# Performance work log

Hardware: AMD Instinct MI355X
Metric: run time of the kernel (lower is better)

Reference implementation:

```python
import jax, jax.numpy as jnp
import numpy as np

TRUNC = (24, 24, 24)
OUT = (32, 32, 32)


def setup_inputs() -> dict:
    key = jax.random.key(0)
    x = jax.random.normal(key, (8, 32, 48, 48, 48), dtype=jnp.float32)
    return {"x": x}


def reference(x):
    # "DCT" as implemented in the source: real part of an ortho-normalized 3D FFT
    x_dct = jnp.real(jnp.fft.fftn(x, axes=(2, 3, 4), norm='ortho'))
    # crop to low-frequency corner, zero-pad up to output_size
    x_crop = x_dct[:, :, :TRUNC[0], :TRUNC[1], :TRUNC[2]]
    pad = ((0, 0), (0, 0),
           (0, OUT[0] - TRUNC[0]),
           (0, OUT[1] - TRUNC[1]),
           (0, OUT[2] - TRUNC[2]))
    x_pad = jnp.pad(x_crop, pad)
    # inverse transform on the output_size grid, keep real part
    x_idct = jnp.real(jnp.fft.ifftn(x_pad, axes=(2, 3, 4), norm='ortho'))
    return x_idct
```

## Files before the change

kernel.cpp:

```cpp
#include <hip/hip_runtime.h>
#include <math.h>


#define TWO_PI_48 0.13089969389957470f
#define TWO_PI_32 0.19634954084936207f
#define NORM_F    1.6611664e-05f

typedef _Float16 half8  __attribute__((ext_vector_type(8)));
typedef _Float16 half4v __attribute__((ext_vector_type(4)));
typedef float    f32x4  __attribute__((ext_vector_type(4)));

__device__ _Float16 T1frag[2][3][2][64][8];
__device__ _Float16 T2frag[2][3][2][64][8];
__device__ __align__(16) _Float16 TK2frag[2][4][3][64][8];
__device__ __align__(16) _Float16 MB2frag[2][4][2][64][8];
__device__ __align__(16) _Float16 TB3frag[2][2][2][64][8];

__device__ int g_twdone = 0;

__global__ void k_init_tw() {
  if (g_twdone) return;
  const int idx = blockIdx.x * 256 + threadIdx.x;
  if (idx < 3072) {
    const int j  = idx & 7;
    const int l  = (idx >> 3) & 63;
    const int ks = (idx >> 9) & 1;
    const int t  = idx >> 10;
    const int k  = ks * 32 + (l >> 4) * 8 + j;
    {
      const int m = t * 16 + (l & 15);
      float v = 0.f;
      if (k < 48) {
        const float a = (float)(((m % 24) * k) % 48) * TWO_PI_48;
        v = (m < 24) ? cosf(a) : -sinf(a);
      }
      const _Float16 h = (_Float16)v;
      T1frag[0][t][ks][l][j] = h;
      T1frag[1][t][ks][l][j] = (_Float16)(v - (float)h);
    }
    {
      const int c = t * 16 + (l & 15);
      float v = 0.f;
      if (k < 48) {
        const float a = (float)(((c % 24) * k) % 48) * TWO_PI_48;
        v = (c < 24) ? cosf(a) : sinf(a);
      }
      const _Float16 h = (_Float16)v;
      T2frag[0][t][ks][l][j] = h;
      T2frag[1][t][ks][l][j] = (_Float16)(v - (float)h);
    }
  } else if (idx < 3072 + 6144) {
    const int local = idx - 3072;
    const int j = local & 7, l = (local >> 3) & 63;
    const int rest = local >> 9;
    const int ks = rest % 3, mt = rest / 3;
    const int m   = mt * 16 + (l & 15);
    const int kap = ks * 32 + (l >> 4) * 8 + j;
    const int n1  = kap % 48;
    const bool isVi = kap >= 48;
    const int m1  = m & 31;
    const bool isWi = m >= 32;
    float acc = 0.f;
    for (int k1 = 0; k1 < 24; ++k1) {
      float s32v, c32v, s48v, c48v;
      sincosf((float)((k1 * m1) % 32) * TWO_PI_32, &s32v, &c32v);
      sincosf((float)((k1 * n1) % 48) * TWO_PI_48, &s48v, &c48v);
      acc = fmaf(isWi ? s32v : c32v, isVi ? s48v : c48v, acc);
    }
    const _Float16 h = (_Float16)acc;
    TK2frag[0][mt][ks][l][j] = h;
    TK2frag[1][mt][ks][l][j] = (_Float16)(acc - (float)h);
  } else if (idx < 3072 + 6144 + 4096) {
    const int local = idx - (3072 + 6144);
    const int j = local & 7, l = (local >> 3) & 63;
    const int rest = local >> 9;
    const int ks = rest & 1, mt = rest >> 1;
    const int m   = mt * 16 + (l & 15);
    const int kap = ks * 32 + (l >> 4) * 8 + j;
    float v = 0.f;
    if (kap < 48) {
      const int k2 = kap % 24;
      const int m2 = m & 31;
      float s, c;
      sincosf((float)((k2 * m2) % 32) * TWO_PI_32, &s, &c);
      if (m < 32) v = (kap < 24) ? c : -s;
      else        v = (kap < 24) ? s :  c;
    }
    const _Float16 h = (_Float16)v;
    MB2frag[0][mt][ks][l][j] = h;
    MB2frag[1][mt][ks][l][j] = (_Float16)(v - (float)h);
  } else if (idx < 15360) {
    const int local = idx - (3072 + 6144 + 4096);
    const int j = local & 7, l = (local >> 3) & 63;
    const int rest = local >> 9;
    const int ks = rest & 1, nt = rest >> 1;
    const int m3  = nt * 16 + (l & 15);
    const int kap = ks * 32 + (l >> 4) * 8 + j;
    float v = 0.f;
    if (kap < 48) {
      const int k3 = kap % 24;
      float s, c;
      sincosf((float)((k3 * m3) % 32) * TWO_PI_32, &s, &c);
      v = (kap < 24) ? c : -s;
    }
    const _Float16 h = (_Float16)v;
    TB3frag[0][nt][ks][l][j] = h;
    TB3frag[1][nt][ks][l][j] = (_Float16)(v - (float)h);
  }
}

__device__ inline void split8(const float* qf, half8& h, half8& lo) {
#pragma unroll
  for (int j = 0; j < 8; ++j) {
    const _Float16 hh = (_Float16)qf[j];
    h[j]  = hh;
    lo[j] = (_Float16)(qf[j] - (float)hh);
  }
}

__global__ __launch_bounds__(192) void k_a12_mfma(const float* __restrict__ x,
                                                  float2* __restrict__ V) {
  const int bx   = blockIdx.x;
  const int bc   = blockIdx.y;
  const int tid  = threadIdx.x;
  const int lane = tid & 63;
  const int w    = tid >> 6;

  __shared__ __align__(16) unsigned char arenaX[13824];
  __shared__ __align__(16) unsigned char arenaU[13824];
  _Float16* Xh = (_Float16*)arenaX;
  _Float16* Xl = (_Float16*)(arenaX + 6912);
  float*    D2 = (float*)arenaX;
  _Float16* Uh = (_Float16*)arenaU;
  _Float16* Ul = (_Float16*)(arenaU + 6912);

  half8 t1h[3][2], t1l[3][2];
#pragma unroll
  for (int mt = 0; mt < 3; ++mt)
#pragma unroll
    for (int ks = 0; ks < 2; ++ks) {
      t1h[mt][ks] = *(const half8*)&T1frag[0][mt][ks][lane][0];
      t1l[mt][ks] = *(const half8*)&T1frag[1][mt][ks][lane][0];
    }
  half8 t2h[2], t2l[2];
#pragma unroll
  for (int ks = 0; ks < 2; ++ks) {
    t2h[ks] = *(const half8*)&T2frag[0][w][ks][lane][0];
    t2l[ks] = *(const half8*)&T2frag[1][w][ks][lane][0];
  }

  if (tid < 96) {
    _Float16* p = (tid < 48 ? Uh : Ul) + (tid % 48) * 72 + 48;
    *(half8*)&p[0] = (half8){};
    *(half8*)&p[8] = (half8){};
  }

  const int kb   = (lane >> 4) * 8;
  const int c16  = lane & 15;
  const int k2e  = tid % 24;
  const int k30e = (tid / 24) * 3;

  float4 xr0, xr1, xr2;
  {
    const float4* g4 = (const float4*)(x + ((size_t)(bc * 48 + bx * 2)) * 2304);
    xr0 = g4[tid]; xr1 = g4[tid + 192]; xr2 = g4[tid + 384];
  }

  for (int g = 0; g < 2; ++g) {
    const int n1 = bx * 2 + g;

    {
      const float4 fr[3] = {xr0, xr1, xr2};
#pragma unroll
      for (int jj = 0; jj < 3; ++jj) {
        const int i4 = tid + 192 * jj;
        const int r = i4 / 12, c4 = i4 % 12;
        const float4 f = fr[jj];
        const _Float16 h0 = (_Float16)f.x, h1 = (_Float16)f.y,
                       h2 = (_Float16)f.z, h3 = (_Float16)f.w;
        const half4v hv = {h0, h1, h2, h3};
        const half4v lv = {(_Float16)(f.x - (float)h0), (_Float16)(f.y - (float)h1),
                           (_Float16)(f.z - (float)h2), (_Float16)(f.w - (float)h3)};
        *(half4v*)&Xh[r * 72 + c4 * 4] = hv;
        *(half4v*)&Xl[r * 72 + c4 * 4] = lv;
      }
    }
    if (tid < 96) {
      _Float16* p = (tid < 48 ? Xh : Xl) + (tid % 48) * 72 + 48;
      *(half8*)&p[0] = (half8){};
      *(half8*)&p[8] = (half8){};
    }
    if (g < 1) {
      const float4* g4 = (const float4*)(x + ((size_t)(bc * 48 + n1 + 1)) * 2304);
      xr0 = g4[tid]; xr1 = g4[tid + 192]; xr2 = g4[tid + 384];
    }
    __syncthreads();

    f32x4 acc0 = {}, acc1 = {}, acc2 = {};
#pragma unroll
    for (int ks = 0; ks < 2; ++ks) {
      const half8 bh = *(const half8*)&Xh[(w * 16 + c16) * 72 + ks * 32 + kb];
      const half8 bl = *(const half8*)&Xl[(w * 16 + c16) * 72 + ks * 32 + kb];
#pragma unroll
      for (int mt = 0; mt < 3; ++mt) {
        f32x4& acc = (mt == 0) ? acc0 : (mt == 1) ? acc1 : acc2;
        acc = __builtin_amdgcn_mfma_f32_16x16x32_f16(t1h[mt][ks], bh, acc, 0, 0, 0);
        acc = __builtin_amdgcn_mfma_f32_16x16x32_f16(t1h[mt][ks], bl, acc, 0, 0, 0);
        acc = __builtin_amdgcn_mfma_f32_16x16x32_f16(t1l[mt][ks], bh, acc, 0, 0, 0);
      }
    }

#pragma unroll
    for (int mt = 0; mt < 3; ++mt) {
      const int r0 = mt * 16 + (lane >> 4) * 4;
      const int cc = w * 16 + c16;
      const f32x4 acc = (mt == 0) ? acc0 : (mt == 1) ? acc1 : acc2;
#pragma unroll
      for (int r = 0; r < 4; ++r) {
        const float v = acc[r];
        const _Float16 h = (_Float16)v;
        Uh[(r0 + r) * 72 + cc] = h;
        Ul[(r0 + r) * 72 + cc] = (_Float16)(v - (float)h);
      }
    }
    __syncthreads();

    f32x4 d20 = {}, d21 = {}, d22 = {};
#pragma unroll
    for (int ks = 0; ks < 2; ++ks) {
#pragma unroll
      for (int mt = 0; mt < 3; ++mt) {
        const half8 ah = *(const half8*)&Uh[(mt * 16 + c16) * 72 + ks * 32 + kb];
        const half8 al = *(const half8*)&Ul[(mt * 16 + c16) * 72 + ks * 32 + kb];
        f32x4& acc = (mt == 0) ? d20 : (mt == 1) ? d21 : d22;
        acc = __builtin_amdgcn_mfma_f32_16x16x32_f16(ah, t2h[ks], acc, 0, 0, 0);
        acc = __builtin_amdgcn_mfma_f32_16x16x32_f16(ah, t2l[ks], acc, 0, 0, 0);
        acc = __builtin_amdgcn_mfma_f32_16x16x32_f16(al, t2h[ks], acc, 0, 0, 0);
      }
    }

#pragma unroll
    for (int mt = 0; mt < 3; ++mt) {
      const int r0 = mt * 16 + (lane >> 4) * 4;
      const int cc = w * 16 + c16;
      const f32x4 acc = (mt == 0) ? d20 : (mt == 1) ? d21 : d22;
#pragma unroll
      for (int r = 0; r < 4; ++r) D2[(r0 + r) * 68 + cc] = acc[r];
    }
    __syncthreads();

    float2* Vp = V + (size_t)(bc * 24) * 1152 + (size_t)n1 * 24 + k2e;
#pragma unroll
    for (int q = 0; q < 3; ++q) {
      const int k3 = k30e + q;
      const float grr = D2[k3 * 68 + k2e];
      const float gis = D2[(k3 + 24) * 68 + k2e + 24];
      const float gir = D2[(k3 + 24) * 68 + k2e];
      const float grs = D2[k3 * 68 + k2e + 24];
      Vp[(size_t)k3 * 1152] = make_float2(grr + gis, gir - grs);
    }
    __syncthreads();
  }
}

__global__ __launch_bounds__(192) void k2_mfma(float2* __restrict__ V) {
  const int k3   = blockIdx.x;
  const int byy  = blockIdx.y;
  const int tid  = threadIdx.x;
  const int lane = tid & 63;
  const int w    = tid >> 6;

  __shared__ __align__(16) float Bb[48 * 100];

  half8 kth[4][3], ktl[4][3];
#pragma unroll
  for (int mt = 0; mt < 4; ++mt)
#pragma unroll
    for (int ks = 0; ks < 3; ++ks) {
      kth[mt][ks] = *(const half8*)&TK2frag[0][mt][ks][lane][0];
      ktl[mt][ks] = *(const half8*)&TK2frag[1][mt][ks][lane][0];
    }

  const int kbase = (lane >> 4) * 8;
  const int c16   = lane & 15;
  const int cc    = w * 16 + c16;
  const int sE    = cc / 24, k2E = cc % 24;
  const int rbase = (lane >> 4) * 4;

  float4 vr[6];
  {
    const float4* g0 = (const float4*)(V + ((size_t)((byy * 4 + 0) * 24 + k3)) * 1152);
    const float4* g1 = (const float4*)(V + ((size_t)((byy * 4 + 1) * 24 + k3)) * 1152);
#pragma unroll
    for (int jj = 0; jj < 6; ++jj)
      vr[jj] = (jj < 3 ? g0 : g1)[tid + 192 * (jj % 3)];
  }

  for (int g = 0; g < 2; ++g) {
    const int bcp = byy * 2 + g;
    float2* slab0 = V + ((size_t)((bcp * 2 + 0) * 24 + k3)) * 1152;
    float2* slab1 = V + ((size_t)((bcp * 2 + 1) * 24 + k3)) * 1152;

    if (g) __syncthreads();

#pragma unroll
    for (int jj = 0; jj < 6; ++jj) {
      const int s = jj / 3;
      const int r = tid + 192 * (jj % 3);
      const int n1 = r / 12, c4 = r % 12;
      const float4 f = vr[jj];
      float* bp = &Bb[(s * 24 + c4 * 2) * 100 + n1];
      bp[0]   = f.x;  bp[48]  = f.y;
      bp[100] = f.z;  bp[148] = f.w;
    }
    if (g < 1) {
      const float4* g0 = (const float4*)(V + ((size_t)((bcp * 2 + 2) * 24 + k3)) * 1152);
      const float4* g1 = (const float4*)(V + ((size_t)((bcp * 2 + 3) * 24 + k3)) * 1152);
#pragma unroll
      for (int jj = 0; jj < 6; ++jj)
        vr[jj] = (jj < 3 ? g0 : g1)[tid + 192 * (jj % 3)];
    }
    __syncthreads();

    f32x4 a0 = {}, a1 = {}, a2 = {}, a3 = {};
#pragma unroll
    for (int ks = 0; ks < 3; ++ks) {
      const float4 q0 = *(const float4*)&Bb[cc * 100 + ks * 32 + kbase];
      const float4 q1 = *(const float4*)&Bb[cc * 100 + ks * 32 + kbase + 4];
      const float qf[8] = {q0.x, q0.y, q0.z, q0.w, q1.x, q1.y, q1.z, q1.w};
      half8 bh, bl;
      split8(qf, bh, bl);
#pragma unroll
      for (int mt = 0; mt < 4; ++mt) {
        f32x4& acc = (mt == 0) ? a0 : (mt == 1) ? a1 : (mt == 2) ? a2 : a3;
        acc = __builtin_amdgcn_mfma_f32_16x16x32_f16(kth[mt][ks], bh, acc, 0, 0, 0);
        acc = __builtin_amdgcn_mfma_f32_16x16x32_f16(kth[mt][ks], bl, acc, 0, 0, 0);
        acc = __builtin_amdgcn_mfma_f32_16x16x32_f16(ktl[mt][ks], bh, acc, 0, 0, 0);
      }
    }

    float2* slab = sE ? slab1 : slab0;
#pragma unroll
    for (int mt = 0; mt < 2; ++mt) {
      const f32x4 wr = (mt == 0) ? a0 : a1;
      const f32x4 wi = (mt == 0) ? a2 : a3;
#pragma unroll
      for (int r = 0; r < 4; ++r) {
        const int m1 = mt * 16 + rbase + r;
        slab[m1 * 24 + k2E] = make_float2(wr[r], wi[r]);
      }
    }
  }
}

__global__ __launch_bounds__(128) void k3_mfma(const float2* __restrict__ V,
                                               float* __restrict__ out) {
  const int m1   = blockIdx.x;
  const int byy  = blockIdx.y;
  const int tid  = threadIdx.x;
  const int lane = tid & 63;
  const int w    = tid >> 6;

  __shared__ __align__(16) float Bt[32 * 68];
  __shared__ __align__(16) float Zb[32 * 68];

  half8 mbh[4][2], mbl[4][2];
#pragma unroll
  for (int mt = 0; mt < 4; ++mt)
#pragma unroll
    for (int ks = 0; ks < 2; ++ks) {
      mbh[mt][ks] = *(const half8*)&MB2frag[0][mt][ks][lane][0];
      mbl[mt][ks] = *(const half8*)&MB2frag[1][mt][ks][lane][0];
    }
  half8 tb3h[2], tb3l[2];
#pragma unroll
  for (int ks = 0; ks < 2; ++ks) {
    tb3h[ks] = *(const half8*)&TB3frag[0][w][ks][lane][0];
    tb3l[ks] = *(const half8*)&TB3frag[1][w][ks][lane][0];
  }

  for (int i = tid; i < 8 * 68; i += 128)  Bt[(24 + i / 68) * 68 + (i % 68)] = 0.f;
  for (int i = tid; i < 24 * 20; i += 128) Bt[(i / 20) * 68 + 48 + (i % 20)] = 0.f;
  for (int i = tid; i < 32 * 20; i += 128) Zb[(i / 20) * 68 + 48 + (i % 20)] = 0.f;

  const int kbase = (lane >> 4) * 8;
  const int c16   = lane & 15;
  const int cc    = w * 16 + c16;
  const int rbase = (lane >> 4) * 4;

  float4 vr0, vr1, vr2;
  {
    const float4* g4 = (const float4*)(V + (size_t)(byy * 2) * 24 * 1152 + (size_t)m1 * 24);
    vr0 = g4[(tid      / 12) * 576 + (tid      % 12)];
    vr1 = g4[((tid+128)/ 12) * 576 + ((tid+128)% 12)];
    if (tid < 32) vr2 = g4[((tid+256)/12) * 576 + ((tid+256)%12)];
  }

  for (int g = 0; g < 2; ++g) {
    const int bc = byy * 2 + g;

    {
      const float4 fr[3] = {vr0, vr1, vr2};
#pragma unroll
      for (int jj = 0; jj < 3; ++jj) {
        const int i4 = tid + 128 * jj;
        if (jj < 2 || tid < 32) {
          const int k3 = i4 / 12, c4 = i4 % 12;
          const float4 f = fr[jj];
          Bt[k3 * 68 + 2 * c4]          = f.x;
          Bt[k3 * 68 + 24 + 2 * c4]     = f.y;
          Bt[k3 * 68 + 2 * c4 + 1]      = f.z;
          Bt[k3 * 68 + 24 + 2 * c4 + 1] = f.w;
        }
      }
    }
    if (g < 1) {
      const float4* g4 = (const float4*)(V + (size_t)(bc + 1) * 24 * 1152 + (size_t)m1 * 24);
      vr0 = g4[(tid      / 12) * 576 + (tid      % 12)];
      vr1 = g4[((tid+128)/ 12) * 576 + ((tid+128)% 12)];
      if (tid < 32) vr2 = g4[((tid+256)/12) * 576 + ((tid+256)%12)];
    }
    __syncthreads();

    f32x4 z0 = {}, z1 = {}, z2 = {}, z3 = {};
#pragma unroll
    for (int ks = 0; ks < 2; ++ks) {
      const float4 q0 = *(const float4*)&Bt[cc * 68 + ks * 32 + kbase];
      const float4 q1 = *(const float4*)&Bt[cc * 68 + ks * 32 + kbase + 4];
      const float qf[8] = {q0.x, q0.y, q0.z, q0.w, q1.x, q1.y, q1.z, q1.w};
      half8 bh, bl;
      split8(qf, bh, bl);
#pragma unroll
      for (int mt = 0; mt < 4; ++mt) {
        f32x4& acc = (mt == 0) ? z0 : (mt == 1) ? z1 : (mt == 2) ? z2 : z3;
        acc = __builtin_amdgcn_mfma_f32_16x16x32_f16(mbh[mt][ks], bh, acc, 0, 0, 0);
        acc = __builtin_amdgcn_mfma_f32_16x16x32_f16(mbh[mt][ks], bl, acc, 0, 0, 0);
        acc = __builtin_amdgcn_mfma_f32_16x16x32_f16(mbl[mt][ks], bh, acc, 0, 0, 0);
      }
    }
    if (cc < 24) {
#pragma unroll
      for (int mt = 0; mt < 4; ++mt) {
        const f32x4 acc = (mt == 0) ? z0 : (mt == 1) ? z1 : (mt == 2) ? z2 : z3;
        const int row0 = mt * 16 + rbase;
#pragma unroll
        for (int r = 0; r < 4; ++r) {
          const int row = row0 + r;
          if (row < 32) Zb[row * 68 + cc]              = acc[r];
          else          Zb[(row - 32) * 68 + 24 + cc]  = acc[r];
        }
      }
    }
    __syncthreads();

    f32x4 o0 = {}, o1 = {};
#pragma unroll
    for (int ks = 0; ks < 2; ++ks) {
#pragma unroll
      for (int mt = 0; mt < 2; ++mt) {
        const float4 q0 = *(const float4*)&Zb[(mt * 16 + c16) * 68 + ks * 32 + kbase];
        const float4 q1 = *(const float4*)&Zb[(mt * 16 + c16) * 68 + ks * 32 + kbase + 4];
        const float qf[8] = {q0.x, q0.y, q0.z, q0.w, q1.x, q1.y, q1.z, q1.w};
        half8 ah, al;
        split8(qf, ah, al);
        f32x4& acc = (mt == 0) ? o0 : o1;
        acc = __builtin_amdgcn_mfma_f32_16x16x32_f16(ah, tb3h[ks], acc, 0, 0, 0);
        acc = __builtin_amdgcn_mfma_f32_16x16x32_f16(ah, tb3l[ks], acc, 0, 0, 0);
        acc = __builtin_amdgcn_mfma_f32_16x16x32_f16(al, tb3h[ks], acc, 0, 0, 0);
      }
    }
    float* op = out + (size_t)(bc * 32 + m1) * 1024;
#pragma unroll
    for (int mt = 0; mt < 2; ++mt) {
      const f32x4 acc = (mt == 0) ? o0 : o1;
#pragma unroll
      for (int r = 0; r < 4; ++r) {
        const int m2 = mt * 16 + rbase + r;
        op[m2 * 32 + cc] = acc[r] * NORM_F;
      }
    }
  }

  if (tid == 0 && blockIdx.x == 0 && blockIdx.y == 0) g_twdone = 1;
}

extern "C" void kernel_launch(void* const* d_in, const int* in_sizes, int n_in,
                              void* d_out, int out_size, void* d_ws, size_t ws_size,
                              hipStream_t stream) {
  const float* x = (const float*)d_in[0];
  float* out = (float*)d_out;
  float2* V = (float2*)d_ws;

  k_init_tw  <<<dim3(60), dim3(256), 0, stream>>>();
  k_a12_mfma <<<dim3(24, 256), dim3(192), 0, stream>>>(x, V);
  k2_mfma    <<<dim3(24, 64), dim3(192), 0, stream>>>(V);
  k3_mfma    <<<dim3(32, 128), dim3(128), 0, stream>>>(V, out);
}
```

Baseline: 81.45 us.

## Write k2 output to separate buffer in k3-friendly layout; ping-pong LDS arenas

k2 now writes its results to a second workspace buffer W instead of back into V in place. W is laid out so that each k3 block reads a contiguous chunk, which turns k3's strided float4 loads into coalesced ones. Separately, k_a12 alternates two LDS arenas between its two iterations and unrolls that loop, which drops the trailing barrier. The cost is a larger workspace footprint, with k2's stores now strided by 576 elements.

```diff
diff --git a/kernel.cpp b/kernel.cpp
--- a/kernel.cpp
+++ b/kernel.cpp
@@ -126,13 +126,8 @@
   const int lane = tid & 63;
   const int w    = tid >> 6;
 
-  __shared__ __align__(16) unsigned char arenaX[13824];
-  __shared__ __align__(16) unsigned char arenaU[13824];
-  _Float16* Xh = (_Float16*)arenaX;
-  _Float16* Xl = (_Float16*)(arenaX + 6912);
-  float*    D2 = (float*)arenaX;
-  _Float16* Uh = (_Float16*)arenaU;
-  _Float16* Ul = (_Float16*)(arenaU + 6912);
+  __shared__ __align__(16) unsigned char arenaA[13824];
+  __shared__ __align__(16) unsigned char arenaB[13824];
 
   half8 t1h[3][2], t1l[3][2];
 #pragma unroll
@@ -147,12 +142,6 @@
   for (int ks = 0; ks < 2; ++ks) {
     t2h[ks] = *(const half8*)&T2frag[0][w][ks][lane][0];
     t2l[ks] = *(const half8*)&T2frag[1][w][ks][lane][0];
-  }
-
-  if (tid < 96) {
-    _Float16* p = (tid < 48 ? Uh : Ul) + (tid % 48) * 72 + 48;
-    *(half8*)&p[0] = (half8){};
-    *(half8*)&p[8] = (half8){};
   }
 
   const int kb   = (lane >> 4) * 8;
@@ -166,8 +155,16 @@
     xr0 = g4[tid]; xr1 = g4[tid + 192]; xr2 = g4[tid + 384];
   }
 
+#pragma unroll
   for (int g = 0; g < 2; ++g) {
     const int n1 = bx * 2 + g;
+    unsigned char* aX = (g == 0) ? arenaA : arenaB;
+    unsigned char* aU = (g == 0) ? arenaB : arenaA;
+    _Float16* Xh = (_Float16*)aX;
+    _Float16* Xl = (_Float16*)(aX + 6912);
+    float*    D2 = (float*)aX;
+    _Float16* Uh = (_Float16*)aU;
+    _Float16* Ul = (_Float16*)(aU + 6912);
 
     {
       const float4 fr[3] = {xr0, xr1, xr2};
@@ -223,6 +220,11 @@
         Ul[(r0 + r) * 72 + cc] = (_Float16)(v - (float)h);
       }
     }
+    if (tid < 96) {
+      _Float16* p = (tid < 48 ? Uh : Ul) + (tid % 48) * 72 + 48;
+      *(half8*)&p[0] = (half8){};
+      *(half8*)&p[8] = (half8){};
+    }
     __syncthreads();
 
     f32x4 d20 = {}, d21 = {}, d22 = {};
@@ -259,11 +261,11 @@
       const float grs = D2[k3 * 68 + k2e + 24];
       Vp[(size_t)k3 * 1152] = make_float2(grr + gis, gir - grs);
     }
-    __syncthreads();
   }
 }
 
-__global__ __launch_bounds__(192) void k2_mfma(float2* __restrict__ V) {
+__global__ __launch_bounds__(192) void k2_mfma(const float2* __restrict__ V,
+                                               float2* __restrict__ W) {
   const int k3   = blockIdx.x;
   const int byy  = blockIdx.y;
   const int tid  = threadIdx.x;
@@ -298,8 +300,6 @@
 
   for (int g = 0; g < 2; ++g) {
     const int bcp = byy * 2 + g;
-    float2* slab0 = V + ((size_t)((bcp * 2 + 0) * 24 + k3)) * 1152;
-    float2* slab1 = V + ((size_t)((bcp * 2 + 1) * 24 + k3)) * 1152;
 
     if (g) __syncthreads();
 
@@ -339,7 +339,8 @@
       }
     }
 
-    float2* slab = sE ? slab1 : slab0;
+    const int bc = bcp * 2 + sE;
+    float2* wp = W + (size_t)bc * 18432 + (size_t)k3 * 24 + k2E;
 #pragma unroll
     for (int mt = 0; mt < 2; ++mt) {
       const f32x4 wr = (mt == 0) ? a0 : a1;
@@ -347,13 +348,13 @@
 #pragma unroll
       for (int r = 0; r < 4; ++r) {
         const int m1 = mt * 16 + rbase + r;
-        slab[m1 * 24 + k2E] = make_float2(wr[r], wi[r]);
+        wp[(size_t)m1 * 576] = make_float2(wr[r], wi[r]);
       }
     }
   }
 }
 
-__global__ __launch_bounds__(128) void k3_mfma(const float2* __restrict__ V,
+__global__ __launch_bounds__(128) void k3_mfma(const float2* __restrict__ W,
                                                float* __restrict__ out) {
   const int m1   = blockIdx.x;
   const int byy  = blockIdx.y;
@@ -390,10 +391,10 @@
 
   float4 vr0, vr1, vr2;
   {
-    const float4* g4 = (const float4*)(V + (size_t)(byy * 2) * 24 * 1152 + (size_t)m1 * 24);
-    vr0 = g4[(tid      / 12) * 576 + (tid      % 12)];
-    vr1 = g4[((tid+128)/ 12) * 576 + ((tid+128)% 12)];
-    if (tid < 32) vr2 = g4[((tid+256)/12) * 576 + ((tid+256)%12)];
+    const float4* g4 = (const float4*)(W + (size_t)(byy * 2) * 18432 + (size_t)m1 * 576);
+    vr0 = g4[tid];
+    vr1 = g4[tid + 128];
+    if (tid < 32) vr2 = g4[tid + 256];
   }
 
   for (int g = 0; g < 2; ++g) {
@@ -415,10 +416,10 @@
       }
     }
     if (g < 1) {
-      const float4* g4 = (const float4*)(V + (size_t)(bc + 1) * 24 * 1152 + (size_t)m1 * 24);
-      vr0 = g4[(tid      / 12) * 576 + (tid      % 12)];
-      vr1 = g4[((tid+128)/ 12) * 576 + ((tid+128)% 12)];
-      if (tid < 32) vr2 = g4[((tid+256)/12) * 576 + ((tid+256)%12)];
+      const float4* g4 = (const float4*)(W + (size_t)(bc + 1) * 18432 + (size_t)m1 * 576);
+      vr0 = g4[tid];
+      vr1 = g4[tid + 128];
+      if (tid < 32) vr2 = g4[tid + 256];
     }
     __syncthreads();
 
@@ -490,9 +491,10 @@
   const float* x = (const float*)d_in[0];
   float* out = (float*)d_out;
   float2* V = (float2*)d_ws;
+  float2* W = (float2*)((char*)d_ws + 56623104);
 
   k_init_tw  <<<dim3(60), dim3(256), 0, stream>>>();
   k_a12_mfma <<<dim3(24, 256), dim3(192), 0, stream>>>(x, V);
-  k2_mfma    <<<dim3(24, 64), dim3(192), 0, stream>>>(V);
-  k3_mfma    <<<dim3(32, 128), dim3(128), 0, stream>>>(V, out);
+  k2_mfma    <<<dim3(24, 64), dim3(192), 0, stream>>>(V, W);
+  k3_mfma    <<<dim3(32, 128), dim3(128), 0, stream>>>(W, out);
 }
```

New measurement: 81.36 us. Within noise of the previous version (-0.1%).
